# Performance work log

Measured on AMD Instinct MI355X. Metric: run time of the kernel, lower is better.

The kernel has to match this reference:

```python
import jax, jax.numpy as jnp
import numpy as np

EMBED_DIM = 1024
NUM_HEADS = 16
HEAD_DIM = EMBED_DIM // NUM_HEADS


def setup_inputs() -> dict:
    key = jax.random.key(0)
    k1, k2, k3, k4 = jax.random.split(key, 4)
    B, S, D = 2, 2048, EMBED_DIM
    x = jax.random.normal(k1, (B, S, D), dtype=jnp.float32)
    xpos = jax.random.randint(k2, (B, S), 0, 2048, dtype=jnp.int32)
    # torch nn.Linear weights: [out_features, in_features]; qkv_bias=False -> no qkv bias
    qkv_w = jax.random.normal(k3, (3 * D, D), dtype=jnp.float32) * (D ** -0.5)
    proj_w = jax.random.normal(k4, (D, D), dtype=jnp.float32) * (D ** -0.5)
    proj_b = jnp.zeros((D,), dtype=jnp.float32)
    return {"x": x, "xpos": xpos, "qkv_w": qkv_w, "proj_w": proj_w, "proj_b": proj_b}


def reference(x, xpos, qkv_w, proj_w, proj_b):
    # rope is None, dropout rates are 0, so xpos is unused and dropout is identity.
    B, S, D = x.shape
    H, hd = NUM_HEADS, D // NUM_HEADS
    scale = hd ** -0.5

    qkv = x @ qkv_w.T                                   # [B, S, 3D]
    qkv = qkv.reshape(B, S, 3, H, hd)
    qkv = jnp.transpose(qkv, (0, 3, 2, 1, 4))           # [B, H, 3, S, hd]
    q, k, v = qkv[:, :, 0], qkv[:, :, 1], qkv[:, :, 2]  # each [B, H, S, hd]

    scores = jnp.einsum("bhqd,bhkd->bhqk", q, k) * scale  # [B, H, S, S]
    probs = jax.nn.softmax(scores, axis=-1)
    out = jnp.einsum("bhqk,bhkd->bhqd", probs, v)         # [B, H, S, hd]

    out = jnp.transpose(out, (0, 2, 1, 3)).reshape(B, S, D)
    out = out @ proj_w.T + proj_b
    return out
```

## Files before the change

kernel.cpp:

```cpp
#include <hip/hip_runtime.h>


typedef __bf16 bf16_8 __attribute__((ext_vector_type(8)));
typedef __bf16 bf16_4 __attribute__((ext_vector_type(4)));
typedef __bf16 bf16_2 __attribute__((ext_vector_type(2)));
typedef float floatx2 __attribute__((ext_vector_type(2)));
typedef float floatx4 __attribute__((ext_vector_type(4)));
typedef float floatx16 __attribute__((ext_vector_type(16)));
typedef unsigned uintx4 __attribute__((ext_vector_type(4)));

#define MFMA16 __builtin_amdgcn_mfma_f32_16x16x32_bf16
#define MFMA32 __builtin_amdgcn_mfma_f32_32x32x16_bf16
#define CSCALE 0.1803368801111204f
#define EXP2R  __builtin_amdgcn_exp2f

__device__ __forceinline__ void gld16(const __bf16* g, __bf16* l) {
    __builtin_amdgcn_global_load_lds(
        (const __attribute__((address_space(1))) void*)g,
        (__attribute__((address_space(3))) void*)l, 16, 0, 0);
}

__device__ __forceinline__ unsigned cvtpk_bf16(float a, float b) {
    unsigned d;
    __asm__("v_cvt_pk_bf16_f32 %0, %1, %2" : "=v"(d) : "v"(a), "v"(b));
    return d;
}

__device__ __forceinline__ void pl32swap(unsigned& a, unsigned& b) {
    __asm__ __volatile__("v_permlane32_swap_b32 %0, %1" : "+v"(a), "+v"(b));
}

__global__ __launch_bounds__(256) void cvt_all(
    const float* __restrict__ x, const float* __restrict__ w1,
    const float* __restrict__ w2,
    __bf16* __restrict__ xb, __bf16* __restrict__ w1b, __bf16* __restrict__ w2b)
{
    const int i = blockIdx.x * 256 + threadIdx.x;
    const float* src; __bf16* dst; int off;
    if (i < (1 << 20))                  { src = x;  dst = xb;  off = i; }
    else if (i < (1 << 20) + 786432)    { src = w1; dst = w1b; off = i - (1 << 20); }
    else                                { src = w2; dst = w2b; off = i - (1 << 20) - 786432; }
    float4 v = ((const float4*)src)[off];
    bf16_4 o;
    o[0] = (__bf16)v.x; o[1] = (__bf16)v.y; o[2] = (__bf16)v.z; o[3] = (__bf16)v.w;
    ((bf16_4*)dst)[off] = o;
}

__global__ __launch_bounds__(512) void qkv_gemm(
    const __bf16* __restrict__ X, const __bf16* __restrict__ W,
    __bf16* __restrict__ q_ws, __bf16* __restrict__ k_ws, __bf16* __restrict__ vt_ws)
{
    __shared__ __align__(16) __bf16 S[2][2][128 * 64];

    const int tid = threadIdx.x, lane = tid & 63, wv = tid >> 6;
    const int quad = lane >> 4, l15 = lane & 15;
    const int wm = (wv >> 2) * 64, wn = (wv & 3) * 32;
    const int m0 = blockIdx.y * 128, n0 = blockIdx.x * 128;
    const int c = n0 >> 10;

    const __bf16* Abase;
    const __bf16* Bbase;
    if (c == 2) { Abase = X + (size_t)m0 * 1024; Bbase = W + (size_t)n0 * 1024; }
    else        { Abase = W + (size_t)n0 * 1024; Bbase = X + (size_t)m0 * 1024; }

    const int srow = tid >> 3, skc = tid & 7;
    const int ssw  = (skc ^ (srow & 7)) * 8;

#define QKV_STAGE(buf, k0)                                                     \
    {                                                                          \
        _Pragma("unroll")                                                      \
        for (int itg = 0; itg < 2; ++itg) {                                    \
            const int cc = itg * 512 + tid;                                    \
            const int row = srow + itg * 64;                                   \
            gld16(Abase + row * 1024 + (k0) + ssw, &S[buf][0][cc * 8]);        \
            gld16(Bbase + row * 1024 + (k0) + ssw, &S[buf][1][cc * 8]);        \
        }                                                                      \
    }

    floatx4 acc[4][2] = {};
    QKV_STAGE(0, 0)
    __syncthreads();

#pragma unroll 1
    for (int kk = 0; kk < 16; ++kk) {
        const int cur = kk & 1;
        if (kk < 15) QKV_STAGE(cur ^ 1, (kk + 1) * 64)

        const __bf16* As = S[cur][0];
        const __bf16* Bs = S[cur][1];
#pragma unroll
        for (int ks = 0; ks < 2; ++ks) {
            bf16_8 af[4], bf[2];
#pragma unroll
            for (int mt = 0; mt < 4; ++mt) {
                int r = wm + mt * 16 + l15;
                af[mt] = *(const bf16_8*)&As[r * 64 + (((ks * 4 + quad) ^ (r & 7)) * 8)];
            }
#pragma unroll
            for (int nt = 0; nt < 2; ++nt) {
                int r = wn + nt * 16 + l15;
                bf[nt] = *(const bf16_8*)&Bs[r * 64 + (((ks * 4 + quad) ^ (r & 7)) * 8)];
            }
#pragma unroll
            for (int mt = 0; mt < 4; ++mt)
#pragma unroll
                for (int nt = 0; nt < 2; ++nt)
                    acc[mt][nt] = MFMA16(af[mt], bf[nt], acc[mt][nt], 0, 0, 0);
        }

        if (kk < 15) {
            __asm__ __volatile__("s_waitcnt vmcnt(0)" ::: "memory");
            __syncthreads();
        }
    }

    if (c == 2) {
#pragma unroll
        for (int mt = 0; mt < 4; ++mt) {
            const int mbase = m0 + wm + mt * 16 + quad * 4;
            const int b = mbase >> 11, key0 = mbase & 2047;
#pragma unroll
            for (int nt = 0; nt < 2; ++nt) {
                const int n = n0 + wn + nt * 16 + l15;
                const int h = (n >> 6) & 15, d = n & 63;
                const int dt = d >> 5, l31v = d & 31;
                bf16_4 pk;
#pragma unroll
                for (int r = 0; r < 4; ++r) pk[r] = (__bf16)acc[mt][nt][r];
                const size_t off =
                    (((size_t)(b * 16 + h) * 32 + (key0 >> 6)) * 2 + dt) * 2048
                    + ((key0 >> 4) & 3) * 512
                    + (((key0 >> 3) & 1) * 32 + l31v) * 8 + (key0 & 7);
                *(bf16_4*)&vt_ws[off] = pk;
            }
        }
    } else {
        const float scale = (c == 1) ? CSCALE : 1.0f;
#pragma unroll
        for (int mt = 0; mt < 4; ++mt) {
            const int nn = n0 + wm + mt * 16 + quad * 4;
            const int h = (nn >> 6) & 15, d0 = nn & 63;
#pragma unroll
            for (int nt = 0; nt < 2; ++nt) {
                const int token = m0 + wn + nt * 16 + l15;
                const int b = token >> 11, key = token & 2047;
                bf16_4 pk;
#pragma unroll
                for (int r = 0; r < 4; ++r) pk[r] = (__bf16)(acc[mt][nt][r] * scale);
                if (c == 0) {
                    *(bf16_4*)&q_ws[((size_t)(b * 16 + h) * 2048 + key) * 64 + d0] = pk;
                } else {
                    const size_t off =
                        (((size_t)(b * 16 + h) * 32 + (key >> 6)) * 2 + ((key >> 5) & 1)) * 2048
                        + (d0 >> 4) * 512
                        + (((d0 >> 3) & 1) * 32 + (key & 31)) * 8 + (d0 & 7);
                    *(bf16_4*)&k_ws[off] = pk;
                }
            }
        }
    }
#undef QKV_STAGE
}

__global__ __launch_bounds__(256) void attn_kernel(
    const __bf16* __restrict__ q_ws, const __bf16* __restrict__ k_ws,
    const __bf16* __restrict__ vt_ws, __bf16* __restrict__ attn_ws)
{
    __shared__ __align__(16) floatx4 comb[2][8][64];
    __shared__ float lcomb[2][64];

    const int tid = threadIdx.x, lane = tid & 63, w = tid >> 6;
    const int l31 = lane & 31, hi = lane >> 5;
    const int qtile = w & 1, keyhalf = w >> 1;

    const int linear = blockIdx.x + (blockIdx.y << 5);
    const int r = linear >> 3;
    const int bh = ((linear & 7) << 2) + (r & 3);
    const int qblk = r >> 2;
    const int q0 = qblk * 64 + qtile * 32;

    const __bf16* __restrict__ qp  = q_ws  + (size_t)bh * (2048 * 64);
    const __bf16* __restrict__ kb0 = k_ws  + (size_t)bh * 131072 + keyhalf * 65536;
    const __bf16* __restrict__ kb1 = kb0 + 2048;
    const __bf16* __restrict__ vb0 = vt_ws + (size_t)bh * 131072 + keyhalf * 65536;
    const __bf16* __restrict__ vb1 = vb0 + 2048;

    const int vo = lane * 8;

    bf16_8 qf[4];
    {
        const int qrow = q0 + l31;
#pragma unroll
        for (int s = 0; s < 4; ++s)
            qf[s] = *(const bf16_8*)&qp[qrow * 64 + s * 16 + hi * 8];
    }

    floatx16 oacc[2] = {};
    floatx2 ls2[4] = {};
    const floatx16 fzero = {};

    bf16_8 ka[8], kb[8], va[8];
#pragma unroll
    for (int u = 0; u < 8; ++u)
        ka[u] = *(const bf16_8*)&(u < 4 ? kb0 : kb1)[vo + (u & 3) * 512];

#define ATTN_TILE(KC, KN, KT)                                                  \
    {                                                                          \
        const int ko  = (KT) * 4096 + vo;                                      \
        const int kon = ko + 4096;                                             \
        _Pragma("unroll")                                                      \
        for (int u = 0; u < 8; ++u)        \
            va[u] = *(const bf16_8*)&(u < 4 ? vb0 : vb1)[ko + (u & 3) * 512];  \
        floatx16 sacc[2];                                                      \
        __builtin_amdgcn_s_setprio(1);                                         \
        sacc[0] = MFMA32(KC[0], qf[0], fzero, 0, 0, 0);                        \
        sacc[1] = MFMA32(KC[4], qf[0], fzero, 0, 0, 0);                        \
        _Pragma("unroll")                                                      \
        for (int s = 1; s < 4; ++s) {                                          \
            sacc[0] = MFMA32(KC[s],     qf[s], sacc[0], 0, 0, 0);              \
            sacc[1] = MFMA32(KC[4 + s], qf[s], sacc[1], 0, 0, 0);              \
        }                                                                      \
        __builtin_amdgcn_s_setprio(0);                                         \
        _Pragma("unroll")                                                      \
        for (int u = 0; u < 8; ++u)                       \
            KN[u] = *(const bf16_8*)&(u < 4 ? kb0 : kb1)[kon + (u & 3) * 512]; \
        unsigned D[2][4][2];                                                   \
        _Pragma("unroll")                                                      \
        for (int t = 0; t < 2; ++t)                                            \
            _Pragma("unroll")                                                  \
            for (int j = 0; j < 4; ++j)                                        \
                _Pragma("unroll")                                              \
                for (int e = 0; e < 2; ++e) {                                  \
                    float pa = EXP2R(sacc[t][j * 4 + e * 2]);                  \
                    float pb = EXP2R(sacc[t][j * 4 + e * 2 + 1]);              \
                    floatx2 p2; p2[0] = pa; p2[1] = pb;                        \
                    ls2[t * 2 + e] += p2;                    \
                    D[t][j][e] = cvtpk_bf16(pa, pb);                           \
                }                                                              \
        __builtin_amdgcn_s_setprio(1);                                         \
        _Pragma("unroll")                                                      \
        for (int s = 0; s < 4; ++s) {                                          \
            const int t = s >> 1, b2 = (s & 1) * 2;                            \
            unsigned x0 = D[t][b2][0], y0 = D[t][b2 + 1][0];                   \
            unsigned x1 = D[t][b2][1], y1 = D[t][b2 + 1][1];                   \
            pl32swap(x0, y0);                                                  \
            pl32swap(x1, y1);                                                  \
            uintx4 uu; uu[0] = x0; uu[1] = x1; uu[2] = y0; uu[3] = y1;         \
            const bf16_8 pf = __builtin_bit_cast(bf16_8, uu);                  \
            oacc[0] = MFMA32(va[s],     pf, oacc[0], 0, 0, 0);                 \
            oacc[1] = MFMA32(va[4 + s], pf, oacc[1], 0, 0, 0);                 \
        }                                                                      \
        __builtin_amdgcn_s_setprio(0);                                         \
    }

#pragma unroll 1
    for (int it = 0; it < 8; ++it) {
        ATTN_TILE(ka, kb, (it * 2))
        ATTN_TILE(kb, ka, (it * 2 + 1))
    }
#undef ATTN_TILE

    const floatx2 lv = (ls2[0] + ls2[1]) + (ls2[2] + ls2[3]);
    const float lsum = lv[0] + lv[1];
    const float lw = lsum + __shfl_xor(lsum, 32, 64);

    if (keyhalf == 1) {
#pragma unroll
        for (int dt = 0; dt < 2; ++dt)
#pragma unroll
            for (int g = 0; g < 4; ++g) {
                floatx4 v4;
#pragma unroll
                for (int r4 = 0; r4 < 4; ++r4) v4[r4] = oacc[dt][g * 4 + r4];
                comb[qtile][dt * 4 + g][lane] = v4;
            }
        lcomb[qtile][lane] = lw;
    }
    __syncthreads();
    if (keyhalf == 0) {
        const int b = bh >> 4, h = bh & 15;
        const float inv_l = 1.0f / (lw + lcomb[qtile][lane]);
        const int token = b * 2048 + q0 + l31;
#pragma unroll
        for (int dt = 0; dt < 2; ++dt)
#pragma unroll
            for (int g = 0; g < 4; ++g) {
                const floatx4 v2 = comb[qtile][dt * 4 + g][lane];
                bf16_4 ok;
#pragma unroll
                for (int r4 = 0; r4 < 4; ++r4)
                    ok[r4] = (__bf16)((oacc[dt][g * 4 + r4] + v2[r4]) * inv_l);
                *(bf16_4*)&attn_ws[(size_t)token * 1024 + h * 64 + dt * 32 + g * 8 + hi * 4] = ok;
            }
    }
}

__device__ __forceinline__ void proj_stage(
    const __bf16* __restrict__ A, const __bf16* __restrict__ Bp,
    int k0, __bf16* As, __bf16* Bs, int tid)
{
#pragma unroll
    for (int it = 0; it < 4; ++it) {
        int cc = it * 256 + tid;
        int row = cc >> 3, kc = cc & 7;
        gld16(A + row * 1024 + k0 + ((kc ^ (row & 7)) * 8), &As[cc * 8]);
    }
#pragma unroll
    for (int it = 0; it < 2; ++it) {
        int cc = it * 256 + tid;
        int row = cc >> 3, kc = cc & 7;
        gld16(Bp + row * 1024 + k0 + ((kc ^ (row & 7)) * 8), &Bs[cc * 8]);
    }
}

__global__ __launch_bounds__(256) void proj_gemm(
    const __bf16* __restrict__ Ain, const __bf16* __restrict__ W,
    const float* __restrict__ bias, float* __restrict__ out)
{
    __shared__ __align__(16) __bf16 As[2][128 * 64];
    __shared__ __align__(16) __bf16 Bs[2][64 * 64];
    floatx4 acc[4][2] = {};
    const int m0 = blockIdx.y * 128, n0 = blockIdx.x * 64;

    const int tid = threadIdx.x, lane = tid & 63, wv = tid >> 6;
    const int quad = lane >> 4, l15 = lane & 15;
    const int wm = (wv >> 1) * 64, wn = (wv & 1) * 32;

    const __bf16* A  = Ain + (size_t)m0 * 1024;
    const __bf16* Bp = W   + (size_t)n0 * 1024;

    proj_stage(A, Bp, 0, As[0], Bs[0], tid);
    __syncthreads();

#pragma unroll 2
    for (int kk = 0; kk < 16; ++kk) {
        const int cur = kk & 1;
        if (kk < 15)
            proj_stage(A, Bp, (kk + 1) * 64, As[cur ^ 1], Bs[cur ^ 1], tid);

        const __bf16* Ab = As[cur];
        const __bf16* Bb = Bs[cur];
#pragma unroll
        for (int ks = 0; ks < 2; ++ks) {
            bf16_8 af[4], bf[2];
#pragma unroll
            for (int mt = 0; mt < 4; ++mt) {
                int r = wm + mt * 16 + l15;
                af[mt] = *(const bf16_8*)&Ab[r * 64 + (((ks * 4 + quad) ^ (r & 7)) * 8)];
            }
#pragma unroll
            for (int nt = 0; nt < 2; ++nt) {
                int r = wn + nt * 16 + l15;
                bf[nt] = *(const bf16_8*)&Bb[r * 64 + (((ks * 4 + quad) ^ (r & 7)) * 8)];
            }
#pragma unroll
            for (int mt = 0; mt < 4; ++mt)
#pragma unroll
                for (int nt = 0; nt < 2; ++nt)
                    acc[mt][nt] = MFMA16(af[mt], bf[nt], acc[mt][nt], 0, 0, 0);
        }

        if (kk < 15) {
            __asm__ __volatile__("s_waitcnt vmcnt(0)" ::: "memory");
            __syncthreads();
        }
    }

    float bv[2];
#pragma unroll
    for (int nt = 0; nt < 2; ++nt) bv[nt] = bias[n0 + wn + nt * 16 + l15];

#pragma unroll
    for (int mt = 0; mt < 4; ++mt) {
        const int m = m0 + wm + mt * 16 + quad * 4;
#pragma unroll
        for (int nt = 0; nt < 2; ++nt) {
            const int n = n0 + wn + nt * 16 + l15;
#pragma unroll
            for (int r = 0; r < 4; ++r)
                out[(size_t)(m + r) * 1024 + n] = acc[mt][nt][r] + bv[nt];
        }
    }
}

extern "C" void kernel_launch(void* const* d_in, const int* in_sizes, int n_in,
                              void* d_out, int out_size, void* d_ws, size_t ws_size,
                              hipStream_t stream)
{
    const float* x      = (const float*)d_in[0];
    const float* qkv_w  = (const float*)d_in[2];
    const float* proj_w = (const float*)d_in[3];
    const float* proj_b = (const float*)d_in[4];
    float* out = (float*)d_out;

    const size_t SZ   = 4096 * 1024;
    const size_t WQKV = 3072 * 1024;
    const size_t WPRJ = 1024 * 1024;

    __bf16* xb      = (__bf16*)d_ws;
    __bf16* qkvwb   = xb + SZ;
    __bf16* projwb  = qkvwb + WQKV;
    __bf16* q_ws    = projwb + WPRJ;
    __bf16* k_ws    = q_ws + SZ;
    __bf16* vt_ws   = k_ws + SZ;
    __bf16* attn_ws = vt_ws + SZ;

    cvt_all<<<dim3(8192), 256, 0, stream>>>(x, qkv_w, proj_w, xb, qkvwb, projwb);
    qkv_gemm  <<<dim3(24, 32), 512, 0, stream>>>(xb, qkvwb, q_ws, k_ws, vt_ws);
    attn_kernel<<<dim3(32, 32), 256, 0, stream>>>(q_ws, k_ws, vt_ws, attn_ws);
    proj_gemm <<<dim3(16, 32), 256, 0, stream>>>(attn_ws, projwb, proj_b, out);
}
```

Before: 183.4 us.

## Stage K/V tiles through double-buffered LDS shared by four query tiles

The attention kernel now uses 512-thread blocks covering 128 queries. K and V^T tiles are loaded once per block into swizzled, double-buffered LDS with global_load_lds, replacing per-wave register loads from a pre-permuted global layout. The QKV GEMM epilogue now writes plain row-major K and transposed V instead of MFMA-fragment-ordered layouts. The aim is to cut redundant global/L2 traffic for K/V, at the cost of LDS reads, a barrier per key tile and fewer blocks.

```diff
diff --git a/kernel.cpp b/kernel.cpp
--- a/kernel.cpp
+++ b/kernel.cpp
@@ -118,23 +118,19 @@
 #pragma unroll
         for (int mt = 0; mt < 4; ++mt) {
             const int mbase = m0 + wm + mt * 16 + quad * 4;
-            const int b = mbase >> 11, key0 = mbase & 2047;
+            const int b = mbase >> 11, s = mbase & 2047;
 #pragma unroll
             for (int nt = 0; nt < 2; ++nt) {
                 const int n = n0 + wn + nt * 16 + l15;
                 const int h = (n >> 6) & 15, d = n & 63;
-                const int dt = d >> 5, l31v = d & 31;
                 bf16_4 pk;
 #pragma unroll
                 for (int r = 0; r < 4; ++r) pk[r] = (__bf16)acc[mt][nt][r];
-                const size_t off =
-                    (((size_t)(b * 16 + h) * 32 + (key0 >> 6)) * 2 + dt) * 2048
-                    + ((key0 >> 4) & 3) * 512
-                    + (((key0 >> 3) & 1) * 32 + l31v) * 8 + (key0 & 7);
-                *(bf16_4*)&vt_ws[off] = pk;
+                *(bf16_4*)&vt_ws[((size_t)(b * 16 + h) * 64 + d) * 2048 + s] = pk;
             }
         }
     } else {
+        __bf16* dst = (c == 0) ? q_ws : k_ws;
         const float scale = (c == 1) ? CSCALE : 1.0f;
 #pragma unroll
         for (int mt = 0; mt < 4; ++mt) {
@@ -143,49 +139,47 @@
 #pragma unroll
             for (int nt = 0; nt < 2; ++nt) {
                 const int token = m0 + wn + nt * 16 + l15;
-                const int b = token >> 11, key = token & 2047;
+                const int b = token >> 11, skey = token & 2047;
                 bf16_4 pk;
 #pragma unroll
                 for (int r = 0; r < 4; ++r) pk[r] = (__bf16)(acc[mt][nt][r] * scale);
-                if (c == 0) {
-                    *(bf16_4*)&q_ws[((size_t)(b * 16 + h) * 2048 + key) * 64 + d0] = pk;
-                } else {
-                    const size_t off =
-                        (((size_t)(b * 16 + h) * 32 + (key >> 6)) * 2 + ((key >> 5) & 1)) * 2048
-                        + (d0 >> 4) * 512
-                        + (((d0 >> 3) & 1) * 32 + (key & 31)) * 8 + (d0 & 7);
-                    *(bf16_4*)&k_ws[off] = pk;
-                }
+                *(bf16_4*)&dst[((size_t)(b * 16 + h) * 2048 + skey) * 64 + d0] = pk;
             }
         }
     }
 #undef QKV_STAGE
 }
 
-__global__ __launch_bounds__(256) void attn_kernel(
+__global__ __launch_bounds__(512, 4) void attn_kernel(
     const __bf16* __restrict__ q_ws, const __bf16* __restrict__ k_ws,
     const __bf16* __restrict__ vt_ws, __bf16* __restrict__ attn_ws)
 {
-    __shared__ __align__(16) floatx4 comb[2][8][64];
-    __shared__ float lcomb[2][64];
+    __shared__ __align__(16) __bf16 Ks [2][2][64 * 64];
+    __shared__ __align__(16) __bf16 Vts[2][2][64 * 64];
 
     const int tid = threadIdx.x, lane = tid & 63, w = tid >> 6;
     const int l31 = lane & 31, hi = lane >> 5;
-    const int qtile = w & 1, keyhalf = w >> 1;
-
-    const int linear = blockIdx.x + (blockIdx.y << 5);
+    const int qtile = w & 3, keyhalf = w >> 2;
+    const int htid = tid & 255;
+
+    const int linear = blockIdx.x + (blockIdx.y << 4);
     const int r = linear >> 3;
     const int bh = ((linear & 7) << 2) + (r & 3);
-    const int qblk = r >> 2;
-    const int q0 = qblk * 64 + qtile * 32;
+    const int qt = r >> 2;
+    const int q0 = qt * 128 + qtile * 32;
 
     const __bf16* __restrict__ qp  = q_ws  + (size_t)bh * (2048 * 64);
-    const __bf16* __restrict__ kb0 = k_ws  + (size_t)bh * 131072 + keyhalf * 65536;
-    const __bf16* __restrict__ kb1 = kb0 + 2048;
-    const __bf16* __restrict__ vb0 = vt_ws + (size_t)bh * 131072 + keyhalf * 65536;
-    const __bf16* __restrict__ vb1 = vb0 + 2048;
-
-    const int vo = lane * 8;
+    const __bf16* __restrict__ kp  = k_ws  + (size_t)bh * (2048 * 64);
+    const __bf16* __restrict__ vtp = vt_ws + (size_t)bh * (64 * 2048);
+    const int koff = keyhalf * 1024;
+
+    const int srow = htid >> 3, skc = htid & 7;
+    const int sw   = (skc ^ (srow & 7)) * 8;
+    const __bf16* kb0 = kp  + (size_t)(koff + srow) * 64 + sw;
+    const __bf16* kb1 = kp  + (size_t)(koff + srow + 32) * 64 + sw;
+    const __bf16* vb0 = vtp + (size_t)srow * 2048 + koff + sw;
+    const __bf16* vb1 = vtp + (size_t)(srow + 32) * 2048 + koff + sw;
+    const int ldsoff = htid * 8;
 
     bf16_8 qf[4];
     {
@@ -199,71 +193,93 @@
     floatx2 ls2[4] = {};
     const floatx16 fzero = {};
 
-    bf16_8 ka[8], kb[8], va[8];
-#pragma unroll
-    for (int u = 0; u < 8; ++u)
-        ka[u] = *(const bf16_8*)&(u < 4 ? kb0 : kb1)[vo + (u & 3) * 512];
-
-#define ATTN_TILE(KC, KN, KT)                                                  \
-    {                                                                          \
-        const int ko  = (KT) * 4096 + vo;                                      \
-        const int kon = ko + 4096;                                             \
-        _Pragma("unroll")                                                      \
-        for (int u = 0; u < 8; ++u)        \
-            va[u] = *(const bf16_8*)&(u < 4 ? vb0 : vb1)[ko + (u & 3) * 512];  \
-        floatx16 sacc[2];                                                      \
-        __builtin_amdgcn_s_setprio(1);                                         \
-        sacc[0] = MFMA32(KC[0], qf[0], fzero, 0, 0, 0);                        \
-        sacc[1] = MFMA32(KC[4], qf[0], fzero, 0, 0, 0);                        \
-        _Pragma("unroll")                                                      \
-        for (int s = 1; s < 4; ++s) {                                          \
-            sacc[0] = MFMA32(KC[s],     qf[s], sacc[0], 0, 0, 0);              \
-            sacc[1] = MFMA32(KC[4 + s], qf[s], sacc[1], 0, 0, 0);              \
-        }                                                                      \
-        __builtin_amdgcn_s_setprio(0);                                         \
-        _Pragma("unroll")                                                      \
-        for (int u = 0; u < 8; ++u)                       \
-            KN[u] = *(const bf16_8*)&(u < 4 ? kb0 : kb1)[kon + (u & 3) * 512]; \
-        unsigned D[2][4][2];                                                   \
-        _Pragma("unroll")                                                      \
-        for (int t = 0; t < 2; ++t)                                            \
-            _Pragma("unroll")                                                  \
-            for (int j = 0; j < 4; ++j)                                        \
-                _Pragma("unroll")                                              \
-                for (int e = 0; e < 2; ++e) {                                  \
-                    float pa = EXP2R(sacc[t][j * 4 + e * 2]);                  \
-                    float pb = EXP2R(sacc[t][j * 4 + e * 2 + 1]);              \
-                    floatx2 p2; p2[0] = pa; p2[1] = pb;                        \
-                    ls2[t * 2 + e] += p2;                    \
-                    D[t][j][e] = cvtpk_bf16(pa, pb);                           \
-                }                                                              \
-        __builtin_amdgcn_s_setprio(1);                                         \
-        _Pragma("unroll")                                                      \
-        for (int s = 0; s < 4; ++s) {                                          \
-            const int t = s >> 1, b2 = (s & 1) * 2;                            \
-            unsigned x0 = D[t][b2][0], y0 = D[t][b2 + 1][0];                   \
-            unsigned x1 = D[t][b2][1], y1 = D[t][b2 + 1][1];                   \
-            pl32swap(x0, y0);                                                  \
-            pl32swap(x1, y1);                                                  \
-            uintx4 uu; uu[0] = x0; uu[1] = x1; uu[2] = y0; uu[3] = y1;         \
-            const bf16_8 pf = __builtin_bit_cast(bf16_8, uu);                  \
-            oacc[0] = MFMA32(va[s],     pf, oacc[0], 0, 0, 0);                 \
-            oacc[1] = MFMA32(va[4 + s], pf, oacc[1], 0, 0, 0);                 \
-        }                                                                      \
-        __builtin_amdgcn_s_setprio(0);                                         \
-    }
+    gld16(kb0, &Ks [keyhalf][0][ldsoff]);
+    gld16(kb1, &Ks [keyhalf][0][ldsoff + 2048]);
+    gld16(vb0, &Vts[keyhalf][0][ldsoff]);
+    gld16(vb1, &Vts[keyhalf][0][ldsoff + 2048]);
+    __syncthreads();
 
 #pragma unroll 1
-    for (int it = 0; it < 8; ++it) {
-        ATTN_TILE(ka, kb, (it * 2))
-        ATTN_TILE(kb, ka, (it * 2 + 1))
-    }
-#undef ATTN_TILE
+    for (int kt = 0; kt < 16; ++kt) {
+        const int cur = kt & 1;
+        if (kt < 15) {
+            const int ko = (kt + 1) * 64;
+            gld16(kb0 + ko * 64, &Ks [keyhalf][cur ^ 1][ldsoff]);
+            gld16(kb1 + ko * 64, &Ks [keyhalf][cur ^ 1][ldsoff + 2048]);
+            gld16(vb0 + ko,      &Vts[keyhalf][cur ^ 1][ldsoff]);
+            gld16(vb1 + ko,      &Vts[keyhalf][cur ^ 1][ldsoff + 2048]);
+        }
+        const __bf16* Kb = Ks [keyhalf][cur];
+        const __bf16* Vb = Vts[keyhalf][cur];
+
+        floatx16 sacc[2];
+        __builtin_amdgcn_s_setprio(1);
+        {
+            const int kc0 = hi;
+            const int r0 = l31, r1 = 32 + l31;
+            bf16_8 kf0 = *(const bf16_8*)&Kb[r0 * 64 + ((kc0 ^ (r0 & 7)) * 8)];
+            bf16_8 kf1 = *(const bf16_8*)&Kb[r1 * 64 + ((kc0 ^ (r1 & 7)) * 8)];
+            sacc[0] = MFMA32(kf0, qf[0], fzero, 0, 0, 0);
+            sacc[1] = MFMA32(kf1, qf[0], fzero, 0, 0, 0);
+        }
+#pragma unroll
+        for (int s = 1; s < 4; ++s) {
+            const int kc = s * 2 + hi;
+#pragma unroll
+            for (int t = 0; t < 2; ++t) {
+                const int row = t * 32 + l31;
+                bf16_8 kf = *(const bf16_8*)&Kb[row * 64 + ((kc ^ (row & 7)) * 8)];
+                sacc[t] = MFMA32(kf, qf[s], sacc[t], 0, 0, 0);
+            }
+        }
+        __builtin_amdgcn_s_setprio(0);
+
+#pragma unroll
+        for (int s = 0; s < 4; ++s) {
+            const int t = s >> 1, b2 = (s & 1) * 2;
+            unsigned Dw[4];
+#pragma unroll
+            for (int jr = 0; jr < 2; ++jr)
+#pragma unroll
+                for (int e = 0; e < 2; ++e) {
+                    const int j = b2 + jr;
+                    float pa = EXP2R(sacc[t][j * 4 + e * 2]);
+                    float pb = EXP2R(sacc[t][j * 4 + e * 2 + 1]);
+                    floatx2 p2; p2[0] = pa; p2[1] = pb;
+                    ls2[t * 2 + e] += p2;
+                    Dw[jr * 2 + e] = cvtpk_bf16(pa, pb);
+                }
+            unsigned x0 = Dw[0], y0 = Dw[2];
+            unsigned x1 = Dw[1], y1 = Dw[3];
+            pl32swap(x0, y0);
+            pl32swap(x1, y1);
+            uintx4 uu; uu[0] = x0; uu[1] = x1; uu[2] = y0; uu[3] = y1;
+            const bf16_8 pf = __builtin_bit_cast(bf16_8, uu);
+            const int kc = s * 2 + hi;
+            __builtin_amdgcn_s_setprio(1);
+#pragma unroll
+            for (int dt = 0; dt < 2; ++dt) {
+                const int drow = dt * 32 + l31;
+                bf16_8 vf = *(const bf16_8*)&Vb[drow * 64 + ((kc ^ (drow & 7)) * 8)];
+                oacc[dt] = MFMA32(vf, pf, oacc[dt], 0, 0, 0);
+            }
+            __builtin_amdgcn_s_setprio(0);
+        }
+
+        if (kt < 15) {
+            __asm__ __volatile__("s_waitcnt vmcnt(0)" ::: "memory");
+            __syncthreads();
+        }
+    }
 
     const floatx2 lv = (ls2[0] + ls2[1]) + (ls2[2] + ls2[3]);
     const float lsum = lv[0] + lv[1];
     const float lw = lsum + __shfl_xor(lsum, 32, 64);
 
+    __syncthreads();
+    floatx4* comb  = (floatx4*)&Ks[0][0][0];
+    float*   lcomb = (float*)&Vts[0][0][0];
+
     if (keyhalf == 1) {
 #pragma unroll
         for (int dt = 0; dt < 2; ++dt)
@@ -272,20 +288,20 @@
                 floatx4 v4;
 #pragma unroll
                 for (int r4 = 0; r4 < 4; ++r4) v4[r4] = oacc[dt][g * 4 + r4];
-                comb[qtile][dt * 4 + g][lane] = v4;
-            }
-        lcomb[qtile][lane] = lw;
+                comb[((qtile * 8 + dt * 4 + g) << 6) + lane] = v4;
+            }
+        lcomb[(qtile << 6) + lane] = lw;
     }
     __syncthreads();
     if (keyhalf == 0) {
         const int b = bh >> 4, h = bh & 15;
-        const float inv_l = 1.0f / (lw + lcomb[qtile][lane]);
+        const float inv_l = 1.0f / (lw + lcomb[(qtile << 6) + lane]);
         const int token = b * 2048 + q0 + l31;
 #pragma unroll
         for (int dt = 0; dt < 2; ++dt)
 #pragma unroll
             for (int g = 0; g < 4; ++g) {
-                const floatx4 v2 = comb[qtile][dt * 4 + g][lane];
+                const floatx4 v2 = comb[((qtile * 8 + dt * 4 + g) << 6) + lane];
                 bf16_4 ok;
 #pragma unroll
                 for (int r4 = 0; r4 < 4; ++r4)
@@ -407,6 +423,6 @@
 
     cvt_all<<<dim3(8192), 256, 0, stream>>>(x, qkv_w, proj_w, xb, qkvwb, projwb);
     qkv_gemm  <<<dim3(24, 32), 512, 0, stream>>>(xb, qkvwb, q_ws, k_ws, vt_ws);
-    attn_kernel<<<dim3(32, 32), 256, 0, stream>>>(q_ws, k_ws, vt_ws, attn_ws);
+    attn_kernel<<<dim3(16, 32), 512, 0, stream>>>(q_ws, k_ws, vt_ws, attn_ws);
     proj_gemm <<<dim3(16, 32), 256, 0, stream>>>(attn_ws, projwb, proj_b, out);
 }
```

Result: faster. 177.5 us (-3.2%).
